# Kernel tuning notes

Measured on AMD Instinct MI355X. Metric: run time of the kernel, lower is better.

The kernel has to match this reference:

```python
import jax, jax.numpy as jnp
import numpy as np
import math

B, P, PIX, D, C = 128, 256, 256, 512, 10
MAX_STEPS, TOL, EPS = 4, 1e-3, 1e-5


def setup_inputs() -> dict:
    key = jax.random.key(0)
    ks = jax.random.split(key, 12)
    pi = math.pi
    return {
        "x": jax.random.normal(ks[0], (B, P, PIX), jnp.float32),
        "Wp": jax.random.normal(ks[1], (D, PIX), jnp.float32) * (1.0 / math.sqrt(PIX)),
        "bp": jnp.zeros((D,), jnp.float32),
        "q_rot": jax.random.uniform(ks[2], (D,), jnp.float32, -pi, pi),
        "k_rot": jax.random.uniform(ks[3], (D,), jnp.float32, -pi, pi),
        "v_rot": jax.random.uniform(ks[4], (D,), jnp.float32, -pi, pi),
        "ff_real": jax.random.normal(ks[5], (D, D), jnp.float32) * (1.0 / math.sqrt(D)),
        "ff_imag": jax.random.uniform(ks[6], (D, D), jnp.float32, -0.01, 0.01),
        "Wr": jax.random.normal(ks[7], (C, D), jnp.float32) * 0.05,
        "br": jnp.zeros((C,), jnp.float32),
        "Wi": jax.random.normal(ks[8], (C, D), jnp.float32) * 0.05,
        "bi": jnp.zeros((C,), jnp.float32),
    }


def _complex_norm(x):
    # normalize magnitude stats over last dim, preserve phase (torch.std uses ddof=1)
    mag = jnp.abs(x)
    mean_mag = jnp.mean(mag, axis=-1, keepdims=True)
    std_mag = jnp.std(mag, axis=-1, keepdims=True, ddof=1)
    norm_mag = (mag - mean_mag) / (std_mag + EPS)
    scale = jnp.tanh(norm_mag) / (mag + EPS)
    return x * scale


def _fro(z):
    return jnp.sqrt(jnp.sum(jnp.abs(z) ** 2))


def _pos_phase():
    pos = jnp.arange(P, dtype=jnp.float32)[:, None]
    dim = jnp.arange(D, dtype=jnp.float32)[None, :]
    freq = 1.0 / (10000.0 ** (dim / D))
    return pos * freq * math.pi  # (P, D)


def reference(x, Wp, bp, q_rot, k_rot, v_rot, ff_real, ff_imag, Wr, br, Wi, bi):
    mag = jnp.tanh(jnp.einsum('bpi,di->bpd', x, Wp) + bp)
    state = mag.astype(jnp.complex64) * jnp.exp(1j * _pos_phase())[None]  # (B,P,D)
    ff = (ff_real + 1j * ff_imag).astype(jnp.complex64)
    eq, ek, ev = jnp.exp(1j * q_rot), jnp.exp(1j * k_rot), jnp.exp(1j * v_rot)
    scale = 8.0 / math.sqrt(D)
    active = jnp.array(True)
    for _ in range(MAX_STEPS):  # fixed small iteration count; updates frozen after convergence
        prev = state
        q, k, v = state * eq, state * ek, state * ev
        interference = jnp.einsum('bpd,bqd->bpq', q, jnp.conj(k))
        attn = jax.nn.softmax(interference.real * scale, axis=-1)
        attn_out = jnp.einsum('bpq,bqd->bpd', attn.astype(jnp.complex64), v)
        new_state = _complex_norm((prev + attn_out) @ ff)
        diff = _fro(new_state - prev) / (_fro(new_state) + 1e-8)
        state = jnp.where(active, new_state, prev)
        active = jnp.logical_and(active, diff >= TOL)
    pooled = jnp.mean(state, axis=1)  # (B,D) complex
    logits = pooled.real @ Wr.T + br + pooled.imag @ Wi.T + bi
    return logits
```

## Files before the change

kernel.cpp:

```cpp
#include <hip/hip_runtime.h>
#include <math.h>

#define BB   128
#define PP   256
#define PIX_ 256
#define DD   512
#define CC   10
#define MTOT (BB*PP)
#define NK   1024
#define KA   2048
#define KB   3072
#define NSLOT (MTOT/4)

static constexpr float SCALE_F = 0.35355339059327373f;
static constexpr float PI_F    = 3.14159265358979323846f;

typedef short bf16x8 __attribute__((ext_vector_type(8)));
typedef float f32x4  __attribute__((ext_vector_type(4)));

__device__ __forceinline__ unsigned short f2bf(float f) {
    union { float f; unsigned u; } v; v.f = f;
    unsigned r = v.u + 0x7FFF + ((v.u >> 16) & 1);
    return (unsigned short)(r >> 16);
}
__device__ __forceinline__ float bf2f(unsigned short h) {
    union { unsigned u; float f; } v; v.u = ((unsigned)h) << 16;
    return v.f;
}

typedef __attribute__((address_space(3))) unsigned lds_u32;
typedef __attribute__((address_space(1))) const unsigned glb_u32;
__device__ __forceinline__ void gl2lds16(const unsigned short* g, short* l) {
    __builtin_amdgcn_global_load_lds((glb_u32*)g, (lds_u32*)l, 16, 0, 0);
}

__global__ void k_setup(const float* __restrict__ q_rot, const float* __restrict__ k_rot,
                        const float* __restrict__ v_rot,
                        float* __restrict__ freq, float* __restrict__ cd, float* __restrict__ sd,
                        float* __restrict__ cv, float* __restrict__ sv,
                        int* __restrict__ active) {
    int t = threadIdx.x;
    if (t < DD) {
        freq[t] = expf(-(float)t * (9.210340371976184f / 512.0f));
        float dl = q_rot[t] - k_rot[t];
        cd[t] = cosf(dl);       sd[t] = sinf(dl);
        cv[t] = cosf(v_rot[t]); sv[t] = sinf(v_rot[t]);
    }
    if (t == 0) *active = 1;
}

__global__ __launch_bounds__(256) void k_prep3(const float* __restrict__ Fr, const float* __restrict__ Fi,
                                               unsigned short* __restrict__ Bt3) {
    const int n = blockIdx.x;
    const int t = threadIdx.x;
    unsigned short* row = Bt3 + (size_t)n * KB;
#pragma unroll
    for (int j4 = 0; j4 < 4; j4++) {
        const int j = j4 * 256 + t;
        float v;
        if (n < 512) v = (j < 512) ? Fr[(size_t)j * DD + n] : -Fi[(size_t)(j - 512) * DD + n];
        else         v = (j < 512) ? Fi[(size_t)j * DD + (n - 512)] : Fr[(size_t)(j - 512) * DD + (n - 512)];
        const unsigned short hi = f2bf(v);
        const unsigned short lo = f2bf(v - bf2f(hi));
        row[j] = hi; row[NK + j] = hi; row[2 * NK + j] = lo;
    }
}

#define SCAT4(TILE, V4) do { TILE[lk+0][lrow]=(V4).x; TILE[lk+1][lrow]=(V4).y; \
                             TILE[lk+2][lrow]=(V4).z; TILE[lk+3][lrow]=(V4).w; } while(0)

__global__ __launch_bounds__(256) void k_init(const float* __restrict__ x,
        const float* __restrict__ Wp, const float* __restrict__ bp,
        const float* __restrict__ freq,
        float* __restrict__ Sr, float* __restrict__ Si) {
    __shared__ float As[16][68];
    __shared__ float Bs[16][68];
    const int bm = blockIdx.y * 64, bn = blockIdx.x * 64;
    const int t = threadIdx.x, tx = t & 15, ty = t >> 4;
    const int lrow = t >> 2, lk = (t & 3) * 4;
    float acc[4][4] = {};
    for (int k0 = 0; k0 < PIX_; k0 += 16) {
        const float4 a4 = *(const float4*)(x  + (size_t)(bm + lrow) * PIX_ + k0 + lk);
        const float4 b4 = *(const float4*)(Wp + (size_t)(bn + lrow) * PIX_ + k0 + lk);
        __syncthreads();
        SCAT4(As, a4);
        SCAT4(Bs, b4);
        __syncthreads();
#pragma unroll
        for (int kk = 0; kk < 16; ++kk) {
            const float4 av = *(const float4*)&As[kk][ty * 4];
            const float4 bv = *(const float4*)&Bs[kk][tx * 4];
            const float a[4] = {av.x, av.y, av.z, av.w};
            const float b[4] = {bv.x, bv.y, bv.z, bv.w};
#pragma unroll
            for (int i = 0; i < 4; i++)
#pragma unroll
                for (int j = 0; j < 4; j++) acc[i][j] = fmaf(a[i], b[j], acc[i][j]);
        }
    }
#pragma unroll
    for (int i = 0; i < 4; i++) {
        const int m = bm + ty * 4 + i;
        const int p = m & 255;
        float4 vr, vi;
        float* pvr = (float*)&vr; float* pvi = (float*)&vi;
#pragma unroll
        for (int j = 0; j < 4; j++) {
            const int d = bn + tx * 4 + j;
            const float mg = tanhf(acc[i][j] + bp[d]);
            const float ph = (float)p * freq[d] * PI_F;
            float sph, cph; sincosf(ph, &sph, &cph);
            pvr[j] = mg * cph; pvi[j] = mg * sph;
        }
        *(float4*)(Sr + (size_t)m * DD + bn + tx * 4) = vr;
        *(float4*)(Si + (size_t)m * DD + bn + tx * 4) = vi;
    }
}

__global__ __launch_bounds__(256) void k_xy(const float* __restrict__ Sr, const float* __restrict__ Si,
        const float* __restrict__ cd, const float* __restrict__ sd,
        unsigned short* __restrict__ X, unsigned short* __restrict__ Y,
        const int* __restrict__ active) {
    if (*active == 0) return;
    const int r = blockIdx.x, t = threadIdx.x;
    const size_t base = (size_t)r * DD + 2 * t;
    const float2 s_r = *(const float2*)(Sr + base);
    const float2 s_i = *(const float2*)(Si + base);
    const float2 c2  = *(const float2*)(cd + 2 * t);
    const float2 s2  = *(const float2*)(sd + 2 * t);
    unsigned short* xr = X + (size_t)r * KA;
    unsigned short* yr = Y + (size_t)r * KA;
    const float srv[2] = {s_r.x, s_r.y}, siv[2] = {s_i.x, s_i.y};
    const float cv_[2] = {c2.x, c2.y},  sv_[2] = {s2.x, s2.y};
    ushort2 xh_r, xh_i, xl_r, xl_i, yh_r, yh_i, yl_r, yl_i;
    unsigned short* o[8] = {(unsigned short*)&xh_r, (unsigned short*)&xh_i,
                            (unsigned short*)&xl_r, (unsigned short*)&xl_i,
                            (unsigned short*)&yh_r, (unsigned short*)&yh_i,
                            (unsigned short*)&yl_r, (unsigned short*)&yl_i};
#pragma unroll
    for (int e = 0; e < 2; e++) {
        const unsigned short hr = f2bf(srv[e]);
        const unsigned short hi_ = f2bf(siv[e]);
        o[0][e] = hr;  o[2][e] = f2bf(srv[e] - bf2f(hr));
        o[1][e] = hi_; o[3][e] = f2bf(siv[e] - bf2f(hi_));
        const float krr = srv[e] * cv_[e] + siv[e] * sv_[e];
        const float kri = siv[e] * cv_[e] - srv[e] * sv_[e];
        const unsigned short yh1 = f2bf(krr);
        const unsigned short yh2 = f2bf(kri);
        o[4][e] = yh1; o[6][e] = f2bf(krr - bf2f(yh1));
        o[5][e] = yh2; o[7][e] = f2bf(kri - bf2f(yh2));
    }
    *(ushort2*)(xr + 2 * t)        = xh_r;
    *(ushort2*)(xr + 512 + 2 * t)  = xh_i;
    *(ushort2*)(xr + 1024 + 2 * t) = xl_r;
    *(ushort2*)(xr + 1536 + 2 * t) = xl_i;
    *(ushort2*)(yr + 2 * t)        = yh_r;
    *(ushort2*)(yr + 512 + 2 * t)  = yh_i;
    *(ushort2*)(yr + 1024 + 2 * t) = yl_r;
    *(ushort2*)(yr + 1536 + 2 * t) = yl_i;
}

__global__ __launch_bounds__(256) void k_score_mfma(const unsigned short* __restrict__ X,
        const unsigned short* __restrict__ Y,
        float* __restrict__ Asc, const int* __restrict__ active) {
    if (*active == 0) return;
    __shared__ short Al[128][32];
    __shared__ short Bl[128][32];
    const int t = threadIdx.x;
    const int w = t >> 6, L = t & 63;
    const int lane15 = L & 15, quad = L >> 4;
    const int bm = blockIdx.y * 128;
    const int bnG = (((int)blockIdx.y >> 1) * 2 + (int)blockIdx.x) * 128;
    const int qb = blockIdx.x * 128;
    const int gr = t >> 2, ch = (t & 3) * 8;
    short* AlW0 = &Al[0][0] + w * 512;
    short* AlW1 = AlW0 + 64 * 32;
    short* BlW0 = &Bl[0][0] + w * 512;
    short* BlW1 = BlW0 + 64 * 32;
    f32x4 acc[2][8] = {};
    for (int k0 = 0; k0 < KB; k0 += 32) {
        const int acol = (k0 < 2048) ? k0 : (k0 - 2048);
        const int bcol = (k0 < 1024) ? k0 : (k0 - 1024);
        __syncthreads();
        gl2lds16(X + (size_t)(bm + gr) * KA      + acol + ch, AlW0);
        gl2lds16(X + (size_t)(bm + 64 + gr) * KA + acol + ch, AlW1);
        gl2lds16(Y + (size_t)(bnG + gr) * KA      + bcol + ch, BlW0);
        gl2lds16(Y + (size_t)(bnG + 64 + gr) * KA + bcol + ch, BlW1);
        __syncthreads();
        bf16x8 bf[8];
#pragma unroll
        for (int tc = 0; tc < 8; tc++)
            bf[tc] = *(const bf16x8*)&Bl[tc * 16 + lane15][quad * 8];
#pragma unroll
        for (int tr = 0; tr < 2; tr++) {
            const bf16x8 af = *(const bf16x8*)&Al[w * 32 + tr * 16 + lane15][quad * 8];
#pragma unroll
            for (int tc = 0; tc < 8; tc++)
                acc[tr][tc] = __builtin_amdgcn_mfma_f32_16x16x32_bf16(af, bf[tc], acc[tr][tc], 0, 0, 0);
        }
    }
#pragma unroll
    for (int tr = 0; tr < 2; tr++)
#pragma unroll
        for (int tc = 0; tc < 8; tc++) {
            const int q = qb + tc * 16 + lane15;
            const int mbase = bm + w * 32 + tr * 16 + quad * 4;
#pragma unroll
            for (int r = 0; r < 4; r++)
                Asc[(size_t)(mbase + r) * PP + q] = acc[tr][tc][r] * SCALE_F;
        }
}

__global__ __launch_bounds__(256) void k_softmax(const float* __restrict__ A,
        unsigned short* __restrict__ Asp, const int* __restrict__ active) {
    if (*active == 0) return;
    const int row = blockIdx.x * 4 + (threadIdx.x >> 6);
    const int lane = threadIdx.x & 63;
    const float* a = A + (size_t)row * PP;
    unsigned short* o = Asp + (size_t)row * 512;
    float v[4];
#pragma unroll
    for (int k = 0; k < 4; k++) v[k] = a[lane + 64 * k];
    float m = fmaxf(fmaxf(v[0], v[1]), fmaxf(v[2], v[3]));
#pragma unroll
    for (int off = 32; off; off >>= 1) m = fmaxf(m, __shfl_xor(m, off, 64));
    float s = 0.f;
#pragma unroll
    for (int k = 0; k < 4; k++) { v[k] = __expf(v[k] - m); s += v[k]; }
#pragma unroll
    for (int off = 32; off; off >>= 1) s += __shfl_xor(s, off, 64);
    const float inv = 1.0f / s;
#pragma unroll
    for (int k = 0; k < 4; k++) {
        const float val = v[k] * inv;
        const unsigned short h = f2bf(val);
        o[lane + 64 * k] = h;
        o[256 + lane + 64 * k] = f2bf(val - bf2f(h));
    }
}

__global__ __launch_bounds__(256) void k_attnout_mfma(const unsigned short* __restrict__ Asp,
        const unsigned short* __restrict__ X,
        const float* __restrict__ Sr, const float* __restrict__ Si,
        const float* __restrict__ cv, const float* __restrict__ sv,
        unsigned short* __restrict__ A2, const int* __restrict__ active) {
    if (*active == 0) return;
    __shared__ short AhT[128][32];
    __shared__ short AlT[128][32];
    __shared__ short BH[128][40];
    __shared__ short BL[128][40];
    const int t = threadIdx.x;
    const int w = t >> 6, L = t & 63;
    const int lane15 = L & 15, quad = L >> 4;
    const int bm = blockIdx.y * 128;
    const int bn = blockIdx.x * 64;
    const int sample = blockIdx.y >> 1;
    const int gr = t >> 2, ch = (t & 3) * 8;
    short* AhW0 = &AhT[0][0] + w * 512;
    short* AhW1 = AhW0 + 64 * 32;
    short* AlW0 = &AlT[0][0] + w * 512;
    short* AlW1 = AlW0 + 64 * 32;
    const int nn = t & 127, kh = t >> 7;
    const unsigned short* Bsrc = X + (size_t)sample * PP * KA
                               + ((nn < 64) ? (bn + nn) : (512 + bn + nn - 64));
    f32x4 acc[2][8] = {};
    for (int q0 = 0; q0 < PP; q0 += 32) {
        __syncthreads();
        gl2lds16(Asp + (size_t)(bm + gr) * 512      + q0 + ch,       AhW0);
        gl2lds16(Asp + (size_t)(bm + 64 + gr) * 512 + q0 + ch,       AhW1);
        gl2lds16(Asp + (size_t)(bm + gr) * 512      + 256 + q0 + ch, AlW0);
        gl2lds16(Asp + (size_t)(bm + 64 + gr) * 512 + 256 + q0 + ch, AlW1);
#pragma unroll
        for (int kg = 0; kg < 2; kg++) {
            const int qb = kh * 16 + kg * 8;
            bf16x8 hh, ll;
#pragma unroll
            for (int j = 0; j < 8; j++) {
                const size_t o = (size_t)(q0 + qb + j) * KA;
                hh[j] = (short)Bsrc[o];
                ll[j] = (short)Bsrc[o + 1024];
            }
            *(bf16x8*)&BH[nn][qb] = hh;
            *(bf16x8*)&BL[nn][qb] = ll;
        }
        __syncthreads();
        bf16x8 bh[8];
#pragma unroll
        for (int tc = 0; tc < 8; tc++)
            bh[tc] = *(const bf16x8*)&BH[tc * 16 + lane15][quad * 8];
        bf16x8 afh[2];
#pragma unroll
        for (int tr = 0; tr < 2; tr++) {
            afh[tr] = *(const bf16x8*)&AhT[w * 32 + tr * 16 + lane15][quad * 8];
            const bf16x8 afl = *(const bf16x8*)&AlT[w * 32 + tr * 16 + lane15][quad * 8];
#pragma unroll
            for (int tc = 0; tc < 8; tc++)
                acc[tr][tc] = __builtin_amdgcn_mfma_f32_16x16x32_bf16(afh[tr], bh[tc], acc[tr][tc], 0, 0, 0);
#pragma unroll
            for (int tc = 0; tc < 8; tc++)
                acc[tr][tc] = __builtin_amdgcn_mfma_f32_16x16x32_bf16(afl, bh[tc], acc[tr][tc], 0, 0, 0);
        }
#pragma unroll
        for (int tc = 0; tc < 8; tc++) {
            const bf16x8 bl = *(const bf16x8*)&BL[tc * 16 + lane15][quad * 8];
            acc[0][tc] = __builtin_amdgcn_mfma_f32_16x16x32_bf16(afh[0], bl, acc[0][tc], 0, 0, 0);
            acc[1][tc] = __builtin_amdgcn_mfma_f32_16x16x32_bf16(afh[1], bl, acc[1][tc], 0, 0, 0);
        }
    }
#pragma unroll
    for (int tr = 0; tr < 2; tr++) {
#pragma unroll
        for (int tc = 0; tc < 4; tc++) {
            const int d = bn + tc * 16 + lane15;
            const float cvd = cv[d], svd = sv[d];
#pragma unroll
            for (int r = 0; r < 4; r++) {
                const int m = bm + w * 32 + tr * 16 + quad * 4 + r;
                const float wr = acc[tr][tc][r];
                const float wi = acc[tr][tc + 4][r];
                const float tr_ = Sr[(size_t)m * DD + d] + (wr * cvd - wi * svd);
                const float ti_ = Si[(size_t)m * DD + d] + (wr * svd + wi * cvd);
                const unsigned short rh = f2bf(tr_);
                const unsigned short ih = f2bf(ti_);
                unsigned short* arow = A2 + (size_t)m * KA;
                arow[d]        = rh;
                arow[512 + d]  = ih;
                arow[1024 + d] = f2bf(tr_ - bf2f(rh));
                arow[1536 + d] = f2bf(ti_ - bf2f(ih));
            }
        }
    }
}

__global__ __launch_bounds__(256) void k_ff_mfma3(const unsigned short* __restrict__ A2,
        const unsigned short* __restrict__ Bt3,
        float* __restrict__ U, const int* __restrict__ active) {
    if (*active == 0) return;
    __shared__ short Al[128][32];
    __shared__ short Bl[128][32];
    const int t = threadIdx.x;
    const int w = t >> 6, L = t & 63;
    const int lane15 = L & 15, quad = L >> 4;
    const int bm = blockIdx.y * 128, bn = blockIdx.x * 128;
    const int gr = t >> 2, ch = (t & 3) * 8;
    short* AlW0 = &Al[0][0] + w * 512;
    short* AlW1 = AlW0 + 64 * 32;
    short* BlW0 = &Bl[0][0] + w * 512;
    short* BlW1 = BlW0 + 64 * 32;
    f32x4 acc[2][8] = {};
    for (int k0 = 0; k0 < KB; k0 += 32) {
        const int acol = (k0 < 2048) ? k0 : (k0 - 2048);
        __syncthreads();
        gl2lds16(A2  + (size_t)(bm + gr) * KA      + acol + ch, AlW0);
        gl2lds16(A2  + (size_t)(bm + 64 + gr) * KA + acol + ch, AlW1);
        gl2lds16(Bt3 + (size_t)(bn + gr) * KB      + k0 + ch,   BlW0);
        gl2lds16(Bt3 + (size_t)(bn + 64 + gr) * KB + k0 + ch,   BlW1);
        __syncthreads();
        bf16x8 bf[8];
#pragma unroll
        for (int tc = 0; tc < 8; tc++)
            bf[tc] = *(const bf16x8*)&Bl[tc * 16 + lane15][quad * 8];
#pragma unroll
        for (int tr = 0; tr < 2; tr++) {
            const bf16x8 af = *(const bf16x8*)&Al[w * 32 + tr * 16 + lane15][quad * 8];
#pragma unroll
            for (int tc = 0; tc < 8; tc++)
                acc[tr][tc] = __builtin_amdgcn_mfma_f32_16x16x32_bf16(af, bf[tc], acc[tr][tc], 0, 0, 0);
        }
    }
#pragma unroll
    for (int tr = 0; tr < 2; tr++)
#pragma unroll
        for (int tc = 0; tc < 8; tc++) {
            const int n = bn + tc * 16 + lane15;
            const int mbase = bm + w * 32 + tr * 16 + quad * 4;
#pragma unroll
            for (int r = 0; r < 4; r++)
                U[(size_t)(mbase + r) * NK + n] = acc[tr][tc][r];
        }
}

__global__ __launch_bounds__(256) void k_norm(const float* __restrict__ U,
        float* __restrict__ Sr, float* __restrict__ Si,
        float* __restrict__ part, const int* __restrict__ active) {
    if (*active == 0) return;
    __shared__ float red[8];
    const int t = threadIdx.x, rt = t >> 6, L = t & 63;
    const int row = blockIdx.x * 4 + rt;
    const size_t ub = (size_t)row * NK;
    const size_t base = (size_t)row * DD;
    const float4 ur0 = *(const float4*)(U + ub + 4 * L);
    const float4 ur1 = *(const float4*)(U + ub + 256 + 4 * L);
    const float4 ui0 = *(const float4*)(U + ub + 512 + 4 * L);
    const float4 ui1 = *(const float4*)(U + ub + 768 + 4 * L);
    const float4 pr0 = *(const float4*)(Sr + base + 4 * L);
    const float4 pr1 = *(const float4*)(Sr + base + 256 + 4 * L);
    const float4 pi0 = *(const float4*)(Si + base + 4 * L);
    const float4 pi1 = *(const float4*)(Si + base + 256 + 4 * L);
    const float urr[8] = {ur0.x, ur0.y, ur0.z, ur0.w, ur1.x, ur1.y, ur1.z, ur1.w};
    const float uii[8] = {ui0.x, ui0.y, ui0.z, ui0.w, ui1.x, ui1.y, ui1.z, ui1.w};
    float mg[8], msum = 0.f;
#pragma unroll
    for (int e = 0; e < 8; e++) {
        mg[e] = sqrtf(urr[e] * urr[e] + uii[e] * uii[e]);
        msum += mg[e];
    }
#pragma unroll
    for (int off = 32; off; off >>= 1) msum += __shfl_xor(msum, off, 64);
    const float mean = msum * (1.0f / 512.0f);
    float vs = 0.f;
#pragma unroll
    for (int e = 0; e < 8; e++) { const float d = mg[e] - mean; vs += d * d; }
#pragma unroll
    for (int off = 32; off; off >>= 1) vs += __shfl_xor(vs, off, 64);
    const float istd = 1.0f / (sqrtf(vs * (1.0f / 511.0f)) + 1e-5f);
    float nr[8], ni[8];
#pragma unroll
    for (int e = 0; e < 8; e++) {
        const float sc = tanhf((mg[e] - mean) * istd) / (mg[e] + 1e-5f);
        nr[e] = urr[e] * sc; ni[e] = uii[e] * sc;
    }
    const float prr[8] = {pr0.x, pr0.y, pr0.z, pr0.w, pr1.x, pr1.y, pr1.z, pr1.w};
    const float pii[8] = {pi0.x, pi0.y, pi0.z, pi0.w, pi1.x, pi1.y, pi1.z, pi1.w};
    float dd = 0.f, nn = 0.f;
#pragma unroll
    for (int e = 0; e < 8; e++) {
        const float dr = nr[e] - prr[e], di = ni[e] - pii[e];
        dd += dr * dr + di * di;
        nn += nr[e] * nr[e] + ni[e] * ni[e];
    }
    *(float4*)(Sr + base + 4 * L)       = make_float4(nr[0], nr[1], nr[2], nr[3]);
    *(float4*)(Sr + base + 256 + 4 * L) = make_float4(nr[4], nr[5], nr[6], nr[7]);
    *(float4*)(Si + base + 4 * L)       = make_float4(ni[0], ni[1], ni[2], ni[3]);
    *(float4*)(Si + base + 256 + 4 * L) = make_float4(ni[4], ni[5], ni[6], ni[7]);
#pragma unroll
    for (int off = 32; off; off >>= 1) {
        dd += __shfl_xor(dd, off, 64);
        nn += __shfl_xor(nn, off, 64);
    }
    if (L == 0) { red[rt] = dd; red[4 + rt] = nn; }
    __syncthreads();
    if (t == 0)
        *(float2*)(part + 2 * blockIdx.x) =
            make_float2(red[0] + red[1] + red[2] + red[3],
                        red[4] + red[5] + red[6] + red[7]);
}

__global__ __launch_bounds__(256) void k_flag(const float* __restrict__ part, int* __restrict__ active) {
    __shared__ float red[8];
    const int t = threadIdx.x, rt = t >> 6, L = t & 63;
    float dd = 0.f, nn = 0.f;
    for (int i = t; i < NSLOT; i += 256) {
        const float2 p = *(const float2*)(part + 2 * i);
        dd += p.x; nn += p.y;
    }
#pragma unroll
    for (int off = 32; off; off >>= 1) {
        dd += __shfl_xor(dd, off, 64);
        nn += __shfl_xor(nn, off, 64);
    }
    if (L == 0) { red[rt] = dd; red[4 + rt] = nn; }
    __syncthreads();
    if (t == 0) {
        const float d = red[0] + red[1] + red[2] + red[3];
        const float n = red[4] + red[5] + red[6] + red[7];
        const float diff = sqrtf(d) / (sqrtf(n) + 1e-8f);
        const int a = *active;
        *active = (a && (diff >= 1e-3f)) ? 1 : 0;
    }
}

__global__ __launch_bounds__(256) void k_pool(const float* __restrict__ Sr, const float* __restrict__ Si,
        float* __restrict__ Pr, float* __restrict__ Pi) {
    const int gid = blockIdx.x * 256 + threadIdx.x;
    const int b = gid >> 9, d = gid & 511;
    const size_t base = (size_t)b * PP * DD + d;
    float sr = 0.f, si = 0.f;
    for (int p = 0; p < PP; p++) {
        sr += Sr[base + (size_t)p * DD];
        si += Si[base + (size_t)p * DD];
    }
    Pr[gid] = sr * (1.0f / 256.0f);
    Pi[gid] = si * (1.0f / 256.0f);
}

__global__ __launch_bounds__(64) void k_logits(const float* __restrict__ Pr, const float* __restrict__ Pi,
        const float* __restrict__ Wr, const float* __restrict__ br,
        const float* __restrict__ Wi, const float* __restrict__ bi,
        float* __restrict__ out) {
    const int b = blockIdx.x;
    const int lane = threadIdx.x;
    for (int c = 0; c < CC; c++) {
        float acc = 0.f;
#pragma unroll
        for (int k = 0; k < 8; k++) {
            const int d = lane + 64 * k;
            acc += Pr[b * DD + d] * Wr[c * DD + d] + Pi[b * DD + d] * Wi[c * DD + d];
        }
#pragma unroll
        for (int off = 32; off; off >>= 1) acc += __shfl_xor(acc, off, 64);
        if (lane == 0) out[b * CC + c] = acc + br[c] + bi[c];
    }
}

extern "C" void kernel_launch(void* const* d_in, const int* in_sizes, int n_in,
                              void* d_out, int out_size, void* d_ws, size_t ws_size,
                              hipStream_t stream) {
    const float* x     = (const float*)d_in[0];
    const float* Wp    = (const float*)d_in[1];
    const float* bp    = (const float*)d_in[2];
    const float* q_rot = (const float*)d_in[3];
    const float* k_rot = (const float*)d_in[4];
    const float* v_rot = (const float*)d_in[5];
    const float* ffr   = (const float*)d_in[6];
    const float* ffi   = (const float*)d_in[7];
    const float* Wr    = (const float*)d_in[8];
    const float* br    = (const float*)d_in[9];
    const float* Wi    = (const float*)d_in[10];
    const float* bi    = (const float*)d_in[11];
    float* out = (float*)d_out;

    float* ws = (float*)d_ws;
    const size_t plane = (size_t)MTOT * DD;
    const size_t sline = (size_t)PP * DD;

    float* freq = ws;
    float* cd   = freq + DD;
    float* sd   = cd + DD;
    float* cv   = sd + DD;
    float* sv   = cv + DD;
    int*   active = (int*)(sv + DD);
    float* Pr = ws + 4096;
    float* Pi = Pr + (size_t)BB * DD;
    float* part = Pi + (size_t)BB * DD;
    float* Sr = part + 2 * NSLOT;
    float* Si = Sr + plane;
    unsigned short* Bt3 = (unsigned short*)(Si + plane);
    float* chunkbase = Si + plane + (size_t)NK * KB / 2;

    const size_t fixed_f = (4096 + 2 * (size_t)BB * DD + 2 * NSLOT) + 2 * plane + (size_t)NK * KB / 2;
    const size_t perC_f = (size_t)PP * NK + (size_t)PP * KA;

    int C = BB;
    while (C > 1 && (fixed_f + (size_t)C * perC_f) * 4ull > ws_size) C >>= 1;

    float* U = chunkbase;
    float* Asc = U;
    unsigned short* Asp = (unsigned short*)(U + (size_t)C * PP * PP);
    unsigned short* X  = (unsigned short*)(U + (size_t)C * PP * NK);
    unsigned short* Y  = X + (size_t)C * PP * KA;
    unsigned short* A2 = Y;

    k_setup<<<1, 512, 0, stream>>>(q_rot, k_rot, v_rot, freq, cd, sd, cv, sv, active);
    k_prep3<<<NK, 256, 0, stream>>>(ffr, ffi, Bt3);
    k_init<<<dim3(DD / 64, MTOT / 64), 256, 0, stream>>>(x, Wp, bp, freq, Sr, Si);

    for (int it = 0; it < 4; ++it) {
        for (int c0 = 0; c0 < BB; c0 += C) {
            float* Sr_c = Sr + (size_t)c0 * sline;
            float* Si_c = Si + (size_t)c0 * sline;
            float* part_c = part + (size_t)c0 * (PP / 4) * 2;
            k_xy<<<C * PP, 256, 0, stream>>>(Sr_c, Si_c, cd, sd, X, Y, active);
            k_score_mfma<<<dim3(2, C * 2), 256, 0, stream>>>(X, Y, Asc, active);
            k_softmax<<<C * PP / 4, 256, 0, stream>>>(Asc, Asp, active);
            k_attnout_mfma<<<dim3(8, C * 2), 256, 0, stream>>>(Asp, X, Sr_c, Si_c, cv, sv, A2, active);
            k_ff_mfma3<<<dim3(NK / 128, C * 2), 256, 0, stream>>>(A2, Bt3, U, active);
            k_norm<<<C * (PP / 4), 256, 0, stream>>>(U, Sr_c, Si_c, part_c, active);
        }
        k_flag<<<1, 256, 0, stream>>>(part, active);
    }

    k_pool<<<BB * DD / 256, 256, 0, stream>>>(Sr, Si, Pr, Pi);
    k_logits<<<BB, 64, 0, stream>>>(Pr, Pi, Wr, br, Wi, bi, out);
}
```

Measured before the change: 3.609 ms.

## Fuse softmax into score GEMM, cut split-bf16 passes, fuse xy packing into norm

Fuses the score GEMM with row softmax so the fp32 score matrix is never written to or read back from global memory. The score and FF GEMMs now use explicit hi/lo bf16 tiles, so the three-term product reads less packed data, and the FF weight matrix shrinks from three K segments to two. When the whole batch fits in one chunk, X/Y packing moves into the norm kernel, removing a separate pass over the state. The fp32 input projection becomes a split-bf16 MFMA GEMM with pre-packed operands. The costs are more LDS per block, larger accumulator register use in the fused score kernel, and aliasing between the U, X and Y buffers, which now share workspace.

```diff
diff --git a/kernel.cpp b/kernel.cpp
--- a/kernel.cpp
+++ b/kernel.cpp
@@ -9,7 +9,7 @@
 #define MTOT (BB*PP)
 #define NK   1024
 #define KA   2048
-#define KB   3072
+#define KB2  2048
 #define NSLOT (MTOT/4)
 
 static constexpr float SCALE_F = 0.35355339059327373f;
@@ -49,11 +49,11 @@
     if (t == 0) *active = 1;
 }
 
-__global__ __launch_bounds__(256) void k_prep3(const float* __restrict__ Fr, const float* __restrict__ Fi,
-                                               unsigned short* __restrict__ Bt3) {
+__global__ __launch_bounds__(256) void k_prep2(const float* __restrict__ Fr, const float* __restrict__ Fi,
+                                               unsigned short* __restrict__ Bt2) {
     const int n = blockIdx.x;
     const int t = threadIdx.x;
-    unsigned short* row = Bt3 + (size_t)n * KB;
+    unsigned short* row = Bt2 + (size_t)n * KB2;
 #pragma unroll
     for (int j4 = 0; j4 < 4; j4++) {
         const int j = j4 * 256 + t;
@@ -61,9 +61,25 @@
         if (n < 512) v = (j < 512) ? Fr[(size_t)j * DD + n] : -Fi[(size_t)(j - 512) * DD + n];
         else         v = (j < 512) ? Fi[(size_t)j * DD + (n - 512)] : Fr[(size_t)(j - 512) * DD + (n - 512)];
         const unsigned short hi = f2bf(v);
-        const unsigned short lo = f2bf(v - bf2f(hi));
-        row[j] = hi; row[NK + j] = hi; row[2 * NK + j] = lo;
-    }
+        row[j] = hi;
+        row[NK + j] = f2bf(v - bf2f(hi));
+    }
+}
+
+__global__ __launch_bounds__(256) void k_packx(const float* __restrict__ x, unsigned short* __restrict__ Xp) {
+    const int r = blockIdx.x, t = threadIdx.x;
+    const float v = x[(size_t)r * PIX_ + t];
+    const unsigned short h = f2bf(v);
+    Xp[(size_t)r * 512 + t] = h;
+    Xp[(size_t)r * 512 + 256 + t] = f2bf(v - bf2f(h));
+}
+
+__global__ __launch_bounds__(256) void k_wpack(const float* __restrict__ Wp, unsigned short* __restrict__ Wt) {
+    const int d = blockIdx.x, t = threadIdx.x;
+    const float v = Wp[(size_t)d * PIX_ + t];
+    const unsigned short h = f2bf(v);
+    Wt[(size_t)d * 512 + t] = h;
+    Wt[(size_t)d * 512 + 256 + t] = f2bf(v - bf2f(h));
 }
 
 #define SCAT4(TILE, V4) do { TILE[lk+0][lrow]=(V4).x; TILE[lk+1][lrow]=(V4).y; \
@@ -117,9 +133,72 @@
     }
 }
 
+__global__ __launch_bounds__(256) void k_init_mfma(const unsigned short* __restrict__ Xp,
+        const unsigned short* __restrict__ Wt, const float* __restrict__ bp,
+        const float* __restrict__ freq,
+        float* __restrict__ Sr, float* __restrict__ Si) {
+    __shared__ short AH[128][32], AL[128][32];
+    __shared__ short BH[128][32], BL[128][32];
+    const int t = threadIdx.x, w = t >> 6, L = t & 63;
+    const int lane15 = L & 15, quad = L >> 4;
+    const int bm = blockIdx.y * 128, bn = blockIdx.x * 128;
+    const int gr = t >> 2, ch = (t & 3) * 8;
+    short* AHw = &AH[0][0] + w * 512;
+    short* ALw = &AL[0][0] + w * 512;
+    short* BHw = &BH[0][0] + w * 512;
+    short* BLw = &BL[0][0] + w * 512;
+    f32x4 acc[2][8] = {};
+    for (int k0 = 0; k0 < 256; k0 += 32) {
+        __syncthreads();
+        gl2lds16(Xp + (size_t)(bm + gr) * 512      + k0 + ch,       AHw);
+        gl2lds16(Xp + (size_t)(bm + 64 + gr) * 512 + k0 + ch,       AHw + 64 * 32);
+        gl2lds16(Xp + (size_t)(bm + gr) * 512      + 256 + k0 + ch, ALw);
+        gl2lds16(Xp + (size_t)(bm + 64 + gr) * 512 + 256 + k0 + ch, ALw + 64 * 32);
+        gl2lds16(Wt + (size_t)(bn + gr) * 512      + k0 + ch,       BHw);
+        gl2lds16(Wt + (size_t)(bn + 64 + gr) * 512 + k0 + ch,       BHw + 64 * 32);
+        gl2lds16(Wt + (size_t)(bn + gr) * 512      + 256 + k0 + ch, BLw);
+        gl2lds16(Wt + (size_t)(bn + 64 + gr) * 512 + 256 + k0 + ch, BLw + 64 * 32);
+        __syncthreads();
+        bf16x8 ah[2], al[2];
+#pragma unroll
+        for (int tr = 0; tr < 2; tr++) {
+            ah[tr] = *(const bf16x8*)&AH[w * 32 + tr * 16 + lane15][quad * 8];
+            al[tr] = *(const bf16x8*)&AL[w * 32 + tr * 16 + lane15][quad * 8];
+        }
+#pragma unroll
+        for (int tc = 0; tc < 8; tc++) {
+            const bf16x8 bh = *(const bf16x8*)&BH[tc * 16 + lane15][quad * 8];
+            acc[0][tc] = __builtin_amdgcn_mfma_f32_16x16x32_bf16(ah[0], bh, acc[0][tc], 0, 0, 0);
+            acc[1][tc] = __builtin_amdgcn_mfma_f32_16x16x32_bf16(ah[1], bh, acc[1][tc], 0, 0, 0);
+            acc[0][tc] = __builtin_amdgcn_mfma_f32_16x16x32_bf16(al[0], bh, acc[0][tc], 0, 0, 0);
+            acc[1][tc] = __builtin_amdgcn_mfma_f32_16x16x32_bf16(al[1], bh, acc[1][tc], 0, 0, 0);
+            const bf16x8 bl = *(const bf16x8*)&BL[tc * 16 + lane15][quad * 8];
+            acc[0][tc] = __builtin_amdgcn_mfma_f32_16x16x32_bf16(ah[0], bl, acc[0][tc], 0, 0, 0);
+            acc[1][tc] = __builtin_amdgcn_mfma_f32_16x16x32_bf16(ah[1], bl, acc[1][tc], 0, 0, 0);
+        }
+    }
+#pragma unroll
+    for (int tr = 0; tr < 2; tr++)
+#pragma unroll
+        for (int tc = 0; tc < 8; tc++) {
+            const int d = bn + tc * 16 + lane15;
+            const float bpd = bp[d];
+            const float fq = freq[d] * PI_F;
+#pragma unroll
+            for (int r = 0; r < 4; r++) {
+                const int m = bm + w * 32 + tr * 16 + quad * 4 + r;
+                const int p = m & 255;
+                const float mg = tanhf(acc[tr][tc][r] + bpd);
+                float sph, cph; sincosf((float)p * fq, &sph, &cph);
+                Sr[(size_t)m * DD + d] = mg * cph;
+                Si[(size_t)m * DD + d] = mg * sph;
+            }
+        }
+}
+
 __global__ __launch_bounds__(256) void k_xy(const float* __restrict__ Sr, const float* __restrict__ Si,
         const float* __restrict__ cd, const float* __restrict__ sd,
-        unsigned short* __restrict__ X, unsigned short* __restrict__ Y,
+        unsigned short* X, unsigned short* Y,
         const int* __restrict__ active) {
     if (*active == 0) return;
     const int r = blockIdx.x, t = threadIdx.x;
@@ -160,82 +239,69 @@
     *(ushort2*)(yr + 1536 + 2 * t) = yl_i;
 }
 
-__global__ __launch_bounds__(256) void k_score_mfma(const unsigned short* __restrict__ X,
+__global__ __launch_bounds__(256) void k_score_sm(const unsigned short* __restrict__ X,
         const unsigned short* __restrict__ Y,
-        float* __restrict__ Asc, const int* __restrict__ active) {
+        unsigned short* __restrict__ Asp, const int* __restrict__ active) {
     if (*active == 0) return;
-    __shared__ short Al[128][32];
-    __shared__ short Bl[128][32];
+    __shared__ short XH[64][32], XL[64][32];
+    __shared__ short YH[256][32], YL[256][32];
     const int t = threadIdx.x;
     const int w = t >> 6, L = t & 63;
     const int lane15 = L & 15, quad = L >> 4;
-    const int bm = blockIdx.y * 128;
-    const int bnG = (((int)blockIdx.y >> 1) * 2 + (int)blockIdx.x) * 128;
-    const int qb = blockIdx.x * 128;
+    const int bm = blockIdx.x * 64;
+    const int yb = ((int)blockIdx.x >> 2) * 256;
     const int gr = t >> 2, ch = (t & 3) * 8;
-    short* AlW0 = &Al[0][0] + w * 512;
-    short* AlW1 = AlW0 + 64 * 32;
-    short* BlW0 = &Bl[0][0] + w * 512;
-    short* BlW1 = BlW0 + 64 * 32;
-    f32x4 acc[2][8] = {};
-    for (int k0 = 0; k0 < KB; k0 += 32) {
-        const int acol = (k0 < 2048) ? k0 : (k0 - 2048);
-        const int bcol = (k0 < 1024) ? k0 : (k0 - 1024);
-        __syncthreads();
-        gl2lds16(X + (size_t)(bm + gr) * KA      + acol + ch, AlW0);
-        gl2lds16(X + (size_t)(bm + 64 + gr) * KA + acol + ch, AlW1);
-        gl2lds16(Y + (size_t)(bnG + gr) * KA      + bcol + ch, BlW0);
-        gl2lds16(Y + (size_t)(bnG + 64 + gr) * KA + bcol + ch, BlW1);
-        __syncthreads();
-        bf16x8 bf[8];
-#pragma unroll
-        for (int tc = 0; tc < 8; tc++)
-            bf[tc] = *(const bf16x8*)&Bl[tc * 16 + lane15][quad * 8];
-#pragma unroll
-        for (int tr = 0; tr < 2; tr++) {
-            const bf16x8 af = *(const bf16x8*)&Al[w * 32 + tr * 16 + lane15][quad * 8];
-#pragma unroll
-            for (int tc = 0; tc < 8; tc++)
-                acc[tr][tc] = __builtin_amdgcn_mfma_f32_16x16x32_bf16(af, bf[tc], acc[tr][tc], 0, 0, 0);
-        }
-    }
-#pragma unroll
-    for (int tr = 0; tr < 2; tr++)
-#pragma unroll
-        for (int tc = 0; tc < 8; tc++) {
-            const int q = qb + tc * 16 + lane15;
-            const int mbase = bm + w * 32 + tr * 16 + quad * 4;
-#pragma unroll
-            for (int r = 0; r < 4; r++)
-                Asc[(size_t)(mbase + r) * PP + q] = acc[tr][tc][r] * SCALE_F;
-        }
-}
-
-__global__ __launch_bounds__(256) void k_softmax(const float* __restrict__ A,
-        unsigned short* __restrict__ Asp, const int* __restrict__ active) {
-    if (*active == 0) return;
-    const int row = blockIdx.x * 4 + (threadIdx.x >> 6);
-    const int lane = threadIdx.x & 63;
-    const float* a = A + (size_t)row * PP;
-    unsigned short* o = Asp + (size_t)row * 512;
-    float v[4];
-#pragma unroll
-    for (int k = 0; k < 4; k++) v[k] = a[lane + 64 * k];
-    float m = fmaxf(fmaxf(v[0], v[1]), fmaxf(v[2], v[3]));
-#pragma unroll
-    for (int off = 32; off; off >>= 1) m = fmaxf(m, __shfl_xor(m, off, 64));
-    float s = 0.f;
-#pragma unroll
-    for (int k = 0; k < 4; k++) { v[k] = __expf(v[k] - m); s += v[k]; }
-#pragma unroll
-    for (int off = 32; off; off >>= 1) s += __shfl_xor(s, off, 64);
-    const float inv = 1.0f / s;
-#pragma unroll
-    for (int k = 0; k < 4; k++) {
-        const float val = v[k] * inv;
-        const unsigned short h = f2bf(val);
-        o[lane + 64 * k] = h;
-        o[256 + lane + 64 * k] = f2bf(val - bf2f(h));
+    short* XHw = &XH[0][0] + w * 512;
+    short* XLw = &XL[0][0] + w * 512;
+    short* YHw = &YH[0][0] + w * 512;
+    short* YLw = &YL[0][0] + w * 512;
+    f32x4 acc[16] = {};
+    for (int k0 = 0; k0 < 1024; k0 += 32) {
+        __syncthreads();
+        gl2lds16(X + (size_t)(bm + gr) * KA + k0 + ch,        XHw);
+        gl2lds16(X + (size_t)(bm + gr) * KA + 1024 + k0 + ch, XLw);
+#pragma unroll
+        for (int s = 0; s < 4; s++) {
+            gl2lds16(Y + (size_t)(yb + s * 64 + gr) * KA + k0 + ch,        YHw + s * 2048);
+            gl2lds16(Y + (size_t)(yb + s * 64 + gr) * KA + 1024 + k0 + ch, YLw + s * 2048);
+        }
+        __syncthreads();
+        const bf16x8 xh = *(const bf16x8*)&XH[w * 16 + lane15][quad * 8];
+        const bf16x8 xl = *(const bf16x8*)&XL[w * 16 + lane15][quad * 8];
+#pragma unroll
+        for (int tc = 0; tc < 16; tc++) {
+            const bf16x8 yh = *(const bf16x8*)&YH[tc * 16 + lane15][quad * 8];
+            acc[tc] = __builtin_amdgcn_mfma_f32_16x16x32_bf16(xh, yh, acc[tc], 0, 0, 0);
+            acc[tc] = __builtin_amdgcn_mfma_f32_16x16x32_bf16(xl, yh, acc[tc], 0, 0, 0);
+            const bf16x8 yl = *(const bf16x8*)&YL[tc * 16 + lane15][quad * 8];
+            acc[tc] = __builtin_amdgcn_mfma_f32_16x16x32_bf16(xh, yl, acc[tc], 0, 0, 0);
+        }
+    }
+#pragma unroll
+    for (int tc = 0; tc < 16; tc++) acc[tc] *= SCALE_F;
+#pragma unroll
+    for (int r = 0; r < 4; r++) {
+        float mx = acc[0][r];
+#pragma unroll
+        for (int tc = 1; tc < 16; tc++) mx = fmaxf(mx, acc[tc][r]);
+#pragma unroll
+        for (int off = 8; off; off >>= 1) mx = fmaxf(mx, __shfl_xor(mx, off, 64));
+        float s = 0.f;
+        float e[16];
+#pragma unroll
+        for (int tc = 0; tc < 16; tc++) { e[tc] = __expf(acc[tc][r] - mx); s += e[tc]; }
+#pragma unroll
+        for (int off = 8; off; off >>= 1) s += __shfl_xor(s, off, 64);
+        const float inv = 1.0f / s;
+        const int row = bm + w * 16 + quad * 4 + r;
+        unsigned short* o = Asp + (size_t)row * 512;
+#pragma unroll
+        for (int tc = 0; tc < 16; tc++) {
+            const float p = e[tc] * inv;
+            const unsigned short h = f2bf(p);
+            o[tc * 16 + lane15] = h;
+            o[256 + tc * 16 + lane15] = f2bf(p - bf2f(h));
+        }
     }
 }
 
@@ -332,40 +398,49 @@
     }
 }
 
-__global__ __launch_bounds__(256) void k_ff_mfma3(const unsigned short* __restrict__ A2,
-        const unsigned short* __restrict__ Bt3,
+__global__ __launch_bounds__(256) void k_ff_mfma2(const unsigned short* __restrict__ A2,
+        const unsigned short* __restrict__ Bt2,
         float* __restrict__ U, const int* __restrict__ active) {
     if (*active == 0) return;
-    __shared__ short Al[128][32];
-    __shared__ short Bl[128][32];
+    __shared__ short AH[128][32], AL[128][32];
+    __shared__ short BH[128][32], BL[128][32];
     const int t = threadIdx.x;
     const int w = t >> 6, L = t & 63;
     const int lane15 = L & 15, quad = L >> 4;
     const int bm = blockIdx.y * 128, bn = blockIdx.x * 128;
     const int gr = t >> 2, ch = (t & 3) * 8;
-    short* AlW0 = &Al[0][0] + w * 512;
-    short* AlW1 = AlW0 + 64 * 32;
-    short* BlW0 = &Bl[0][0] + w * 512;
-    short* BlW1 = BlW0 + 64 * 32;
+    short* AHw = &AH[0][0] + w * 512;
+    short* ALw = &AL[0][0] + w * 512;
+    short* BHw = &BH[0][0] + w * 512;
+    short* BLw = &BL[0][0] + w * 512;
     f32x4 acc[2][8] = {};
-    for (int k0 = 0; k0 < KB; k0 += 32) {
-        const int acol = (k0 < 2048) ? k0 : (k0 - 2048);
-        __syncthreads();
-        gl2lds16(A2  + (size_t)(bm + gr) * KA      + acol + ch, AlW0);
-        gl2lds16(A2  + (size_t)(bm + 64 + gr) * KA + acol + ch, AlW1);
-        gl2lds16(Bt3 + (size_t)(bn + gr) * KB      + k0 + ch,   BlW0);
-        gl2lds16(Bt3 + (size_t)(bn + 64 + gr) * KB + k0 + ch,   BlW1);
-        __syncthreads();
-        bf16x8 bf[8];
-#pragma unroll
-        for (int tc = 0; tc < 8; tc++)
-            bf[tc] = *(const bf16x8*)&Bl[tc * 16 + lane15][quad * 8];
+    for (int k0 = 0; k0 < 1024; k0 += 32) {
+        __syncthreads();
+        gl2lds16(A2  + (size_t)(bm + gr) * KA       + k0 + ch,        AHw);
+        gl2lds16(A2  + (size_t)(bm + 64 + gr) * KA  + k0 + ch,        AHw + 64 * 32);
+        gl2lds16(A2  + (size_t)(bm + gr) * KA       + 1024 + k0 + ch, ALw);
+        gl2lds16(A2  + (size_t)(bm + 64 + gr) * KA  + 1024 + k0 + ch, ALw + 64 * 32);
+        gl2lds16(Bt2 + (size_t)(bn + gr) * KB2      + k0 + ch,        BHw);
+        gl2lds16(Bt2 + (size_t)(bn + 64 + gr) * KB2 + k0 + ch,        BHw + 64 * 32);
+        gl2lds16(Bt2 + (size_t)(bn + gr) * KB2      + 1024 + k0 + ch, BLw);
+        gl2lds16(Bt2 + (size_t)(bn + 64 + gr) * KB2 + 1024 + k0 + ch, BLw + 64 * 32);
+        __syncthreads();
+        bf16x8 ah[2], al[2];
 #pragma unroll
         for (int tr = 0; tr < 2; tr++) {
-            const bf16x8 af = *(const bf16x8*)&Al[w * 32 + tr * 16 + lane15][quad * 8];
-#pragma unroll
-            for (int tc = 0; tc < 8; tc++)
-                acc[tr][tc] = __builtin_amdgcn_mfma_f32_16x16x32_bf16(af, bf[tc], acc[tr][tc], 0, 0, 0);
+            ah[tr] = *(const bf16x8*)&AH[w * 32 + tr * 16 + lane15][quad * 8];
+            al[tr] = *(const bf16x8*)&AL[w * 32 + tr * 16 + lane15][quad * 8];
+        }
+#pragma unroll
+        for (int tc = 0; tc < 8; tc++) {
+            const bf16x8 bh = *(const bf16x8*)&BH[tc * 16 + lane15][quad * 8];
+            acc[0][tc] = __builtin_amdgcn_mfma_f32_16x16x32_bf16(ah[0], bh, acc[0][tc], 0, 0, 0);
+            acc[1][tc] = __builtin_amdgcn_mfma_f32_16x16x32_bf16(ah[1], bh, acc[1][tc], 0, 0, 0);
+            acc[0][tc] = __builtin_amdgcn_mfma_f32_16x16x32_bf16(al[0], bh, acc[0][tc], 0, 0, 0);
+            acc[1][tc] = __builtin_amdgcn_mfma_f32_16x16x32_bf16(al[1], bh, acc[1][tc], 0, 0, 0);
+            const bf16x8 bl = *(const bf16x8*)&BL[tc * 16 + lane15][quad * 8];
+            acc[0][tc] = __builtin_amdgcn_mfma_f32_16x16x32_bf16(ah[0], bl, acc[0][tc], 0, 0, 0);
+            acc[1][tc] = __builtin_amdgcn_mfma_f32_16x16x32_bf16(ah[1], bl, acc[1][tc], 0, 0, 0);
         }
     }
 #pragma unroll
@@ -380,9 +455,12 @@
         }
 }
 
-__global__ __launch_bounds__(256) void k_norm(const float* __restrict__ U,
+__global__ __launch_bounds__(256) void k_norm(const float* U,
         float* __restrict__ Sr, float* __restrict__ Si,
-        float* __restrict__ part, const int* __restrict__ active) {
+        float* __restrict__ part,
+        unsigned short* X, unsigned short* Y,
+        const float* __restrict__ cd, const float* __restrict__ sd,
+        const int wxy, const int* __restrict__ active) {
     if (*active == 0) return;
     __shared__ float red[8];
     const int t = threadIdx.x, rt = t >> 6, L = t & 63;
@@ -433,6 +511,43 @@
     *(float4*)(Sr + base + 256 + 4 * L) = make_float4(nr[4], nr[5], nr[6], nr[7]);
     *(float4*)(Si + base + 4 * L)       = make_float4(ni[0], ni[1], ni[2], ni[3]);
     *(float4*)(Si + base + 256 + 4 * L) = make_float4(ni[4], ni[5], ni[6], ni[7]);
+    if (wxy) {
+        unsigned short* xr = X + (size_t)row * KA;
+        unsigned short* yr = Y + (size_t)row * KA;
+        const float4 c0 = *(const float4*)(cd + 4 * L);
+        const float4 c1 = *(const float4*)(cd + 256 + 4 * L);
+        const float4 s0 = *(const float4*)(sd + 4 * L);
+        const float4 s1 = *(const float4*)(sd + 256 + 4 * L);
+        const float cdv[8] = {c0.x, c0.y, c0.z, c0.w, c1.x, c1.y, c1.z, c1.w};
+        const float sdv[8] = {s0.x, s0.y, s0.z, s0.w, s1.x, s1.y, s1.z, s1.w};
+        ushort4 xhr[2], xhi[2], xlr[2], xli[2], yhr[2], yhi[2], ylr[2], yli[2];
+#pragma unroll
+        for (int e = 0; e < 8; e++) {
+            const int g = e >> 2, j = e & 3;
+            const unsigned short hr = f2bf(nr[e]);
+            const unsigned short hi_ = f2bf(ni[e]);
+            ((unsigned short*)&xhr[g])[j] = hr;
+            ((unsigned short*)&xlr[g])[j] = f2bf(nr[e] - bf2f(hr));
+            ((unsigned short*)&xhi[g])[j] = hi_;
+            ((unsigned short*)&xli[g])[j] = f2bf(ni[e] - bf2f(hi_));
+            const float krr = nr[e] * cdv[e] + ni[e] * sdv[e];
+            const float kri = ni[e] * cdv[e] - nr[e] * sdv[e];
+            const unsigned short k1 = f2bf(krr);
+            const unsigned short k2 = f2bf(kri);
+            ((unsigned short*)&yhr[g])[j] = k1;
+            ((unsigned short*)&ylr[g])[j] = f2bf(krr - bf2f(k1));
+            ((unsigned short*)&yhi[g])[j] = k2;
+            ((unsigned short*)&yli[g])[j] = f2bf(kri - bf2f(k2));
+        }
+        *(ushort4*)(xr + 4 * L)        = xhr[0]; *(ushort4*)(xr + 256 + 4 * L)  = xhr[1];
+        *(ushort4*)(xr + 512 + 4 * L)  = xhi[0]; *(ushort4*)(xr + 768 + 4 * L)  = xhi[1];
+        *(ushort4*)(xr + 1024 + 4 * L) = xlr[0]; *(ushort4*)(xr + 1280 + 4 * L) = xlr[1];
+        *(ushort4*)(xr + 1536 + 4 * L) = xli[0]; *(ushort4*)(xr + 1792 + 4 * L) = xli[1];
+        *(ushort4*)(yr + 4 * L)        = yhr[0]; *(ushort4*)(yr + 256 + 4 * L)  = yhr[1];
+        *(ushort4*)(yr + 512 + 4 * L)  = yhi[0]; *(ushort4*)(yr + 768 + 4 * L)  = yhi[1];
+        *(ushort4*)(yr + 1024 + 4 * L) = ylr[0]; *(ushort4*)(yr + 1280 + 4 * L) = ylr[1];
+        *(ushort4*)(yr + 1536 + 4 * L) = yli[0]; *(ushort4*)(yr + 1792 + 4 * L) = yli[1];
+    }
 #pragma unroll
     for (int off = 32; off; off >>= 1) {
         dd += __shfl_xor(dd, off, 64);
@@ -535,37 +650,47 @@
     float* part = Pi + (size_t)BB * DD;
     float* Sr = part + 2 * NSLOT;
     float* Si = Sr + plane;
-    unsigned short* Bt3 = (unsigned short*)(Si + plane);
-    float* chunkbase = Si + plane + (size_t)NK * KB / 2;
-
-    const size_t fixed_f = (4096 + 2 * (size_t)BB * DD + 2 * NSLOT) + 2 * plane + (size_t)NK * KB / 2;
-    const size_t perC_f = (size_t)PP * NK + (size_t)PP * KA;
+    unsigned short* Bt2 = (unsigned short*)(Si + plane);
+    unsigned short* Wt  = Bt2 + (size_t)NK * KB2;
+    float* chunkbase = Si + plane + (size_t)NK * 3072 / 2;
+
+    const size_t fixed_f = (4096 + 2 * (size_t)BB * DD + 2 * NSLOT) + 2 * plane + (size_t)NK * 3072 / 2;
+    const size_t perC_f = (size_t)PP * NK * 2 + (size_t)PP * 256;
 
     int C = BB;
     while (C > 1 && (fixed_f + (size_t)C * perC_f) * 4ull > ws_size) C >>= 1;
+    const int fullXY = (C == BB);
+    const int mfmaInit = (C >= 32);
 
     float* U = chunkbase;
-    float* Asc = U;
-    unsigned short* Asp = (unsigned short*)(U + (size_t)C * PP * PP);
-    unsigned short* X  = (unsigned short*)(U + (size_t)C * PP * NK);
-    unsigned short* Y  = X + (size_t)C * PP * KA;
+    unsigned short* X  = (unsigned short*)chunkbase;
+    float* Yf = chunkbase + (size_t)C * PP * NK;
+    unsigned short* Y  = (unsigned short*)Yf;
     unsigned short* A2 = Y;
+    unsigned short* Asp = (unsigned short*)(Yf + (size_t)C * PP * NK);
+    unsigned short* Xp = (unsigned short*)chunkbase;
 
     k_setup<<<1, 512, 0, stream>>>(q_rot, k_rot, v_rot, freq, cd, sd, cv, sv, active);
-    k_prep3<<<NK, 256, 0, stream>>>(ffr, ffi, Bt3);
-    k_init<<<dim3(DD / 64, MTOT / 64), 256, 0, stream>>>(x, Wp, bp, freq, Sr, Si);
+    k_prep2<<<NK, 256, 0, stream>>>(ffr, ffi, Bt2);
+    if (mfmaInit) {
+        k_packx<<<MTOT, 256, 0, stream>>>(x, Xp);
+        k_wpack<<<DD, 256, 0, stream>>>(Wp, Wt);
+        k_init_mfma<<<dim3(DD / 128, MTOT / 128), 256, 0, stream>>>(Xp, Wt, bp, freq, Sr, Si);
+    } else {
+        k_init<<<dim3(DD / 64, MTOT / 64), 256, 0, stream>>>(x, Wp, bp, freq, Sr, Si);
+    }
 
     for (int it = 0; it < 4; ++it) {
         for (int c0 = 0; c0 < BB; c0 += C) {
             float* Sr_c = Sr + (size_t)c0 * sline;
             float* Si_c = Si + (size_t)c0 * sline;
             float* part_c = part + (size_t)c0 * (PP / 4) * 2;
-            k_xy<<<C * PP, 256, 0, stream>>>(Sr_c, Si_c, cd, sd, X, Y, active);
-            k_score_mfma<<<dim3(2, C * 2), 256, 0, stream>>>(X, Y, Asc, active);
-            k_softmax<<<C * PP / 4, 256, 0, stream>>>(Asc, Asp, active);
+            if (!fullXY || it == 0)
+                k_xy<<<C * PP, 256, 0, stream>>>(Sr_c, Si_c, cd, sd, X, Y, active);
+            k_score_sm<<<C * 4, 256, 0, stream>>>(X, Y, Asp, active);
             k_attnout_mfma<<<dim3(8, C * 2), 256, 0, stream>>>(Asp, X, Sr_c, Si_c, cv, sv, A2, active);
-            k_ff_mfma3<<<dim3(NK / 128, C * 2), 256, 0, stream>>>(A2, Bt3, U, active);
-            k_norm<<<C * (PP / 4), 256, 0, stream>>>(U, Sr_c, Si_c, part_c, active);
+            k_ff_mfma2<<<dim3(NK / 128, C * 2), 256, 0, stream>>>(A2, Bt2, U, active);
+            k_norm<<<C * (PP / 4), 256, 0, stream>>>(U, Sr_c, Si_c, part_c, X, Y, cd, sd, fullXY, active);
         }
         k_flag<<<1, 256, 0, stream>>>(part, active);
     }
```

After: 3.268 ms. 1.1x faster.
